# Performance work log

Hardware: AMD Instinct MI355X
Metric: run time of the kernel (lower is better)

Reference implementation:

```python
import jax, jax.numpy as jnp
import numpy as np

NUM_LEVELS = 3
K = 512
COMMIT = (0.25, 0.5, 1.0)
DECAY = 0.99
EPS = 1e-05


def setup_inputs() -> dict:
    key = jax.random.key(0)
    k1, k2, k3 = jax.random.split(key, 3)
    z_e = jax.random.normal(k1, (16, 4096, 1024), dtype=jnp.float32)
    codebooks = jax.random.normal(k2, (NUM_LEVELS, K, 1024), dtype=jnp.float32)
    ema_cluster = jnp.ones((NUM_LEVELS, K), dtype=jnp.float32)
    ema_w = jax.random.normal(k3, (NUM_LEVELS, K, 1024), dtype=jnp.float32)
    return {"z_e": z_e, "codebooks": codebooks, "ema_cluster": ema_cluster, "ema_w": ema_w}


def reference(z_e, codebooks, ema_cluster, ema_w):
    """Hierarchical residual VQ: 3 levels of cdist+argmin+gather, residual subtract,
    commitment loss, and EMA codebook update stats via scatter-add (segment_sum)."""
    B, T, D = z_e.shape
    flat = z_e.reshape(-1, D)  # [N, D]
    residual = flat
    z_q = jnp.zeros_like(flat)
    loss = jnp.zeros((), dtype=flat.dtype)
    idx_list = []
    new_codebooks = []

    for l in range(NUM_LEVELS):
        C = codebooks[l]  # [K, D]
        # squared euclidean distances [N, K] (expanded form, no NxKxD intermediate)
        d = (jnp.sum(residual * residual, axis=-1, keepdims=True)
             - 2.0 * residual @ C.T
             + jnp.sum(C * C, axis=-1))
        idx = jnp.argmin(d, axis=-1)  # [N] nearest code
        q = C[idx]  # gather [N, D]

        # commitment loss (EMA-style VQ: no gradient codebook loss)
        loss = loss + COMMIT[l] * jnp.mean((residual - jax.lax.stop_gradient(q)) ** 2)

        # EMA codebook update statistics (scatter-add, no grad)
        r_sg = jax.lax.stop_gradient(residual)
        counts = jax.ops.segment_sum(jnp.ones((r_sg.shape[0],), dtype=flat.dtype), idx, num_segments=K)
        sums = jax.ops.segment_sum(r_sg, idx, num_segments=K)  # [K, D]
        cs = DECAY * ema_cluster[l] + (1.0 - DECAY) * counts
        w = DECAY * ema_w[l] + (1.0 - DECAY) * sums
        n = jnp.sum(cs)
        cs_norm = (cs + EPS) / (n + K * EPS) * n  # laplace smoothing
        new_codebooks.append(w / cs_norm[:, None])

        residual = residual - q
        z_q = z_q + q
        idx_list.append(idx)

    # straight-through estimator
    z_q_st = flat + jax.lax.stop_gradient(z_q - flat)
    indices = jnp.stack(idx_list).reshape(NUM_LEVELS, B, T)
    return z_q_st.reshape(B, T, D), loss, indices, jnp.stack(new_codebooks)
```

## Files before the change

kernel.cpp:

```cpp
#include <hip/hip_runtime.h>

#define NPTS   65536
#define DIM    1024
#define NCODE  512
#define NLVL   3

#define ZQ_OFF   0
#define LOSS_OFF 67108864
#define IDX_OFF  67108865
#define CB_OFF   67305473

#define PB    128
#define CBCH  256
#define KS    64
#define NTHR2 512

typedef unsigned short u16;
typedef unsigned int   u32;
typedef __attribute__((ext_vector_type(8))) short short8;
typedef __attribute__((ext_vector_type(4))) float f32x4;

__device__ inline void merge_top2(float& v1, int& i1, float& v2, int& i2,
                                  float w1, int j1, float w2, int j2) {
    bool aFirst = (v1 < w1) || (v1 == w1 && i1 < j1);
    float t1v = aFirst ? v1 : w1; int t1i = aFirst ? i1 : j1;
    float c1v = aFirst ? v2 : w2; int c1i = aFirst ? i2 : j2;
    float c2v = aFirst ? w1 : v1; int c2i = aFirst ? j1 : i1;
    bool cFirst = (c1v < c2v) || (c1v == c2v && c1i < c2i);
    v1 = t1v; i1 = t1i;
    v2 = cFirst ? c1v : c2v;
    i2 = cFirst ? c1i : c2i;
}

__device__ inline u16 bf16_rne(float x) {
    u32 u = __float_as_uint(x);
    u32 r = u + 0x7fffu + ((u >> 16) & 1u);
    return (u16)(r >> 16);
}
__device__ inline float bf16_f(u16 h) { return __uint_as_float(((u32)h) << 16); }

__device__ inline void gload_lds16(const void* g, void* l) {
    __builtin_amdgcn_global_load_lds((const __attribute__((address_space(1))) void*)g,
                                     (__attribute__((address_space(3))) void*)l, 16, 0, 0);
}

__global__ __launch_bounds__(256) void cnorm_kernel(const float* __restrict__ cb,
                                                    float* __restrict__ cnorm) {
    __shared__ float sd[256];
    const int b = blockIdx.x;
    const int tid = threadIdx.x;
    const float4 v = *(const float4*)&cb[(size_t)b * DIM + tid * 4];
    sd[tid] = v.x*v.x + v.y*v.y + v.z*v.z + v.w*v.w;
    __syncthreads();
    for (int o = 128; o > 0; o >>= 1) { if (tid < o) sd[tid] += sd[tid+o]; __syncthreads(); }
    if (tid == 0) cnorm[b] = sd[0];
}

__global__ __launch_bounds__(256) void cvtcb_kernel(const float* __restrict__ cbs,
                                                    char* __restrict__ planes) {
    const int b = blockIdx.x;
    const int tid = threadIdx.x;
    const int l = b >> 9, k = b & 511;
    u16* ph = (u16*)(planes + (size_t)l * 2097152);
    u16* pl = ph + NCODE * DIM;
    const float4 v = *(const float4*)&cbs[(size_t)b * DIM + tid * 4];
    float xs[4] = {v.x, v.y, v.z, v.w};
    u16 hh[4], ll[4];
    #pragma unroll
    for (int e = 0; e < 4; ++e) {
        hh[e] = bf16_rne(xs[e]);
        ll[e] = bf16_rne(xs[e] - bf16_f(hh[e]));
    }
    *(ushort4*)&ph[(size_t)k * DIM + tid * 4] = make_ushort4(hh[0], hh[1], hh[2], hh[3]);
    *(ushort4*)&pl[(size_t)k * DIM + tid * 4] = make_ushort4(ll[0], ll[1], ll[2], ll[3]);
}

__global__ __launch_bounds__(512, 2) void level_kernel(
        const float* __restrict__ r_in,
        float* __restrict__ r_out,
        const float* __restrict__ cbf,
        const u16* __restrict__ cb_h,
        const u16* __restrict__ cb_l,
        const float* __restrict__ cnorm_l,
        float* __restrict__ out_idx_f,
        int*   __restrict__ ws_idx,
        float* __restrict__ loss_partial)
{
    __shared__ u16 sA[2][CBCH][KS];
    __shared__ u16 sB[2][PB][KS];
    __shared__ float s_cn[NCODE];
    __shared__ float4 s_top[4][PB];
    __shared__ int s_i1[PB], s_i2[PB], s_w[PB];
    __shared__ double s_ref[PB][2][2];
    __shared__ float s_red[NTHR2];

    const int tid  = threadIdx.x;
    const int lane = tid & 63;
    const int wid  = tid >> 6;
    const int wm   = wid >> 1;
    const int wn   = wid & 1;
    const int g    = lane >> 4;
    const int l15  = lane & 15;
    const int pbase = blockIdx.x * PB;

    u16* sAf = &sA[0][0][0];
    u16* sBf = &sB[0][0][0];

    s_cn[tid] = cnorm_l[tid];

    float bv1[4], bv2[4]; int bi1[4], bi2[4];
    #pragma unroll
    for (int i = 0; i < 4; ++i) { bv1[i] = 1e30f; bv2[i] = 1e30f; bi1[i] = 0; bi2[i] = 1; }

    const u16* srcp = (wid < 4) ? cb_h : cb_l;

    for (int ch = 0; ch < 2; ++ch) {
        const int cbase = ch * CBCH;
        f32x4 acc[4][4] = {};

        for (int ks0 = 0; ks0 < DIM; ks0 += KS) {
            __syncthreads();

            #pragma unroll
            for (int j = 0; j < 8; ++j) {
                const int cbk = wid * 512 + j * 64;
                const int c   = cbk + lane;
                const int cc  = c & 2047;
                const int row = cc >> 3, slot = cc & 7;
                const u16* gp = srcp + (size_t)(cbase + row) * DIM + ks0
                                + ((slot ^ (row & 7)) << 3);
                gload_lds16(gp, sAf + (size_t)cbk * 8);
            }

            #pragma unroll
            for (int j = 0; j < 2; ++j) {
                const int s = tid + j * 512;
                const int row = s >> 3, slot = s & 7;
                const float* gp = r_in + (size_t)(pbase + row) * DIM + ks0 + slot * 8;
                const float4 a0 = *(const float4*)gp;
                const float4 a1 = *(const float4*)(gp + 4);
                float xs[8] = {a0.x, a0.y, a0.z, a0.w, a1.x, a1.y, a1.z, a1.w};
                short8 h8, l8;
                #pragma unroll
                for (int e = 0; e < 8; ++e) {
                    const u16 hb = bf16_rne(xs[e]);
                    const u16 lb = bf16_rne(xs[e] - bf16_f(hb));
                    h8[e] = (short)hb; l8[e] = (short)lb;
                }
                const int woff = row * KS + ((slot ^ (row & 7)) << 3);
                *(short8*)(sBf + woff) = h8;
                *(short8*)(sBf + 8192 + woff) = l8;
            }
            asm volatile("s_waitcnt vmcnt(0)" ::: "memory");
            __syncthreads();

            #pragma unroll
            for (int ksub = 0; ksub < 2; ++ksub) {
                const int rsw = (((ksub << 2) + g) ^ (lane & 7)) << 3;
                short8 bh[4], bl[4];
                #pragma unroll
                for (int nf = 0; nf < 4; ++nf) {
                    const int row = wn * 64 + nf * 16 + l15;
                    bh[nf] = *(const short8*)(sBf + row * KS + rsw);
                    bl[nf] = *(const short8*)(sBf + 8192 + row * KS + rsw);
                }
                #pragma unroll
                for (int mf = 0; mf < 4; ++mf) {
                    const int row = wm * 64 + mf * 16 + l15;
                    const short8 ah = *(const short8*)(sAf + row * KS + rsw);
                    const short8 al = *(const short8*)(sAf + 16384 + row * KS + rsw);
                    #pragma unroll
                    for (int nf = 0; nf < 4; ++nf) {
                        acc[mf][nf] = __builtin_amdgcn_mfma_f32_16x16x32_bf16(ah, bh[nf], acc[mf][nf], 0, 0, 0);
                        acc[mf][nf] = __builtin_amdgcn_mfma_f32_16x16x32_bf16(ah, bl[nf], acc[mf][nf], 0, 0, 0);
                        acc[mf][nf] = __builtin_amdgcn_mfma_f32_16x16x32_bf16(al, bh[nf], acc[mf][nf], 0, 0, 0);
                    }
                }
            }
        }

        #pragma unroll
        for (int nf = 0; nf < 4; ++nf)
            #pragma unroll
            for (int mf = 0; mf < 4; ++mf)
                #pragma unroll
                for (int r = 0; r < 4; ++r) {
                    const int code = cbase + wm * 64 + mf * 16 + g * 4 + r;
                    const float sv = s_cn[code] - 2.0f * acc[mf][nf][r];
                    if (sv < bv1[nf])      { bv2[nf] = bv1[nf]; bi2[nf] = bi1[nf]; bv1[nf] = sv; bi1[nf] = code; }
                    else if (sv < bv2[nf]) { bv2[nf] = sv; bi2[nf] = code; }
                }
    }

    #pragma unroll
    for (int nf = 0; nf < 4; ++nf) {
        float v1 = bv1[nf], v2 = bv2[nf]; int i1 = bi1[nf], i2 = bi2[nf];
        #pragma unroll
        for (int m = 16; m < 64; m <<= 1) {
            const float w1 = __shfl_xor(v1, m); const int j1 = __shfl_xor(i1, m);
            const float w2 = __shfl_xor(v2, m); const int j2 = __shfl_xor(i2, m);
            merge_top2(v1, i1, v2, i2, w1, j1, w2, j2);
        }
        if (g == 0)
            s_top[wm][wn * 64 + nf * 16 + l15] =
                make_float4(v1, __int_as_float(i1), v2, __int_as_float(i2));
    }
    __syncthreads();

    if (tid < PB) {
        float4 t = s_top[0][tid];
        float v1 = t.x; int i1 = __float_as_int(t.y);
        float v2 = t.z; int i2 = __float_as_int(t.w);
        #pragma unroll
        for (int wmm = 1; wmm < 4; ++wmm) {
            const float4 u = s_top[wmm][tid];
            merge_top2(v1, i1, v2, i2, u.x, __float_as_int(u.y), u.z, __float_as_int(u.w));
        }
        s_i1[tid] = i1; s_i2[tid] = i2;
    }
    __syncthreads();

    {
        const int p = tid >> 2, cand = (tid >> 1) & 1, half = tid & 1;
        const int k = cand ? s_i2[p] : s_i1[p];
        const float* rr = r_in + (size_t)(pbase + p) * DIM + half * 512;
        const float* cr = cbf + (size_t)k * DIM + half * 512;
        double s = 0.0;
        for (int d = 0; d < 512; ++d) {
            const double c = (double)cr[d];
            const double r = (double)rr[d];
            s += c * (c - 2.0 * r);
        }
        s_ref[p][cand][half] = s;
    }
    __syncthreads();
    if (tid < PB) {
        const double sA_ = s_ref[tid][0][0] + s_ref[tid][0][1];
        const double sB_ = s_ref[tid][1][0] + s_ref[tid][1][1];
        const int iA = s_i1[tid], iB = s_i2[tid];
        const int w = (sB_ < sA_ || (sB_ == sA_ && iB < iA)) ? iB : iA;
        s_w[tid] = w;
        out_idx_f[pbase + tid] = (float)w;
        ws_idx[pbase + tid] = w;
    }
    __syncthreads();

    float lsum = 0.f;
    const int colb = (tid & 255) * 4;
    const int phh  = tid >> 8;
    for (int pp = 0; pp < PB; pp += 2) {
        const int p = pp + phh;
        const int w = s_w[p];
        const size_t off = (size_t)(pbase + p) * DIM + colb;
        const float4 rv = *(const float4*)&r_in[off];
        const float4 cv = *(const float4*)&cbf[(size_t)w * DIM + colb];
        float4 rn;
        rn.x = rv.x - cv.x; rn.y = rv.y - cv.y; rn.z = rv.z - cv.z; rn.w = rv.w - cv.w;
        if (r_out) *(float4*)&r_out[off] = rn;
        lsum += rn.x*rn.x + rn.y*rn.y + rn.z*rn.z + rn.w*rn.w;
    }
    s_red[tid] = lsum;
    __syncthreads();
    for (int o = 256; o > 0; o >>= 1) { if (tid < o) s_red[tid] += s_red[tid + o]; __syncthreads(); }
    if (tid == 0) loss_partial[blockIdx.x] = s_red[0];
}

#define SCHUNK 4096
__global__ __launch_bounds__(256) void sums_kernel(
        const int* __restrict__ idx, const float* __restrict__ src,
        const float* __restrict__ cb, int addC,
        float* __restrict__ sums_out, int* __restrict__ counts_out)
{
    __shared__ int s_idx[SCHUNK];
    __shared__ int s_list[SCHUNK];
    __shared__ int s_scan[256];
    const int k = blockIdx.x, tid = threadIdx.x;
    float4 acc = make_float4(0.f, 0.f, 0.f, 0.f);
    int nk = 0;
    for (int base = 0; base < NPTS; base += SCHUNK) {
        __syncthreads();
        for (int j = tid; j < SCHUNK; j += 256) s_idx[j] = idx[base + j];
        __syncthreads();
        int cnt = 0;
        const int S = SCHUNK / 256;
        #pragma unroll
        for (int j = 0; j < S; ++j) cnt += (s_idx[tid * S + j] == k);
        s_scan[tid] = cnt;
        __syncthreads();
        for (int off = 1; off < 256; off <<= 1) {
            int v = (tid >= off) ? s_scan[tid - off] : 0;
            __syncthreads();
            s_scan[tid] += v;
            __syncthreads();
        }
        const int total = s_scan[255];
        int pos = s_scan[tid] - cnt;
        for (int j = 0; j < S; ++j)
            if (s_idx[tid * S + j] == k) s_list[pos++] = base + tid * S + j;
        __syncthreads();
        for (int j = 0; j < total; ++j) {
            const int pid = s_list[j];
            float4 v = *(const float4*)&src[(size_t)pid * DIM + tid * 4];
            acc.x += v.x; acc.y += v.y; acc.z += v.z; acc.w += v.w;
        }
        nk += total;
    }
    if (addC) {
        float4 c = *(const float4*)&cb[(size_t)k * DIM + tid * 4];
        float fn = (float)nk;
        acc.x += fn * c.x; acc.y += fn * c.y; acc.z += fn * c.z; acc.w += fn * c.w;
    }
    *(float4*)&sums_out[(size_t)k * DIM + tid * 4] = acc;
    if (tid == 0) counts_out[k] = nk;
}

__global__ __launch_bounds__(256) void zq_kernel(const float* __restrict__ z_e,
                                                 const float* __restrict__ cb2,
                                                 const int* __restrict__ idx2,
                                                 float* __restrict__ zq) {
    const int total = NPTS * (DIM / 4);
    for (int i = blockIdx.x * 256 + threadIdx.x; i < total; i += gridDim.x * 256) {
        const size_t e = (size_t)i * 4;
        const int p = (int)(e >> 10);
        const int d = (int)(e & 1023);
        const int w = idx2[p];
        float4 z = *(const float4*)&z_e[e];
        float4 r = *(const float4*)&zq[e];
        float4 c = *(const float4*)&cb2[(size_t)w * DIM + d];
        float4 o;
        o.x = z.x - r.x + c.x; o.y = z.y - r.y + c.y;
        o.z = z.z - r.z + c.z; o.w = z.w - r.w + c.w;
        *(float4*)&zq[e] = o;
    }
}

__global__ __launch_bounds__(512) void nsum_kernel(const float* __restrict__ ec,
                                                   const int* __restrict__ counts,
                                                   float* __restrict__ n_ws) {
    __shared__ float sd[512];
    const int l = blockIdx.x, tid = threadIdx.x;
    sd[tid] = 0.99f * ec[l * NCODE + tid] + 0.01f * (float)counts[l * NCODE + tid];
    __syncthreads();
    for (int o = 256; o > 0; o >>= 1) { if (tid < o) sd[tid] += sd[tid+o]; __syncthreads(); }
    if (tid == 0) n_ws[l] = sd[0];
}

__global__ __launch_bounds__(256) void newcb_kernel(const float* __restrict__ ema_w,
                                                    const float* __restrict__ sums,
                                                    const float* __restrict__ ec,
                                                    const int* __restrict__ counts,
                                                    const float* __restrict__ n_ws,
                                                    float* __restrict__ out_cb) {
    const int b = blockIdx.x;
    const int tid = threadIdx.x;
    const int l = b >> 9;
    const float cs = 0.99f * ec[b] + 0.01f * (float)counts[b];
    const float n = n_ws[l];
    const float csn = (cs + 1e-5f) / (n + 512.0f * 1e-5f) * n;
    const size_t off = (size_t)b * DIM + tid * 4;
    float4 w = *(const float4*)&ema_w[off];
    float4 s4 = *(const float4*)&sums[off];
    float4 o;
    o.x = (0.99f * w.x + 0.01f * s4.x) / csn;
    o.y = (0.99f * w.y + 0.01f * s4.y) / csn;
    o.z = (0.99f * w.z + 0.01f * s4.z) / csn;
    o.w = (0.99f * w.w + 0.01f * s4.w) / csn;
    *(float4*)&out_cb[off] = o;
}

__global__ __launch_bounds__(256) void loss_kernel(const float* __restrict__ lp,
                                                   float* __restrict__ out_loss) {
    __shared__ double sd[256];
    const int tid = threadIdx.x;
    const double commit[3] = {0.25, 0.5, 1.0};
    double acc = 0.0;
    for (int l = 0; l < NLVL; ++l) {
        double s = 0.0;
        for (int j = tid; j < 512; j += 256) s += (double)lp[l * 512 + j];
        sd[tid] = s;
        __syncthreads();
        for (int o = 128; o > 0; o >>= 1) { if (tid < o) sd[tid] += sd[tid+o]; __syncthreads(); }
        if (tid == 0) acc += commit[l] * sd[0] / 67108864.0;
        __syncthreads();
    }
    if (tid == 0) *out_loss = (float)acc;
}

extern "C" void kernel_launch(void* const* d_in, const int* in_sizes, int n_in,
                              void* d_out, int out_size, void* d_ws, size_t ws_size,
                              hipStream_t stream) {
    const float* z_e   = (const float*)d_in[0];
    const float* cbs   = (const float*)d_in[1];
    const float* ema_c = (const float*)d_in[2];
    const float* ema_w = (const float*)d_in[3];
    float* out = (float*)d_out;

    char* ws = (char*)d_ws;
    int*   ws_idx = (int*)ws;
    float* cnorm  = (float*)(ws + 786432);
    int*   counts = (int*)(ws + 792576);
    float* lossp  = (float*)(ws + 798720);
    float* n_ws   = (float*)(ws + 811008);
    float* sums   = (float*)(ws + 811024);
    char*  planes = (char*)(ws + 811024);

    float* zq       = out + ZQ_OFF;
    float* out_loss = out + LOSS_OFF;
    float* out_idx  = out + IDX_OFF;
    float* out_cb   = out + CB_OFF;

    const float* cb0 = cbs;
    const float* cb1 = cbs + (size_t)1 * NCODE * DIM;
    const float* cb2 = cbs + (size_t)2 * NCODE * DIM;

    u16* ph0 = (u16*)(planes);                     u16* pl0 = ph0 + NCODE * DIM;
    u16* ph1 = (u16*)(planes + 2097152);           u16* pl1 = ph1 + NCODE * DIM;
    u16* ph2 = (u16*)(planes + 2 * 2097152);       u16* pl2 = ph2 + NCODE * DIM;

    cvtcb_kernel<<<NLVL * NCODE, 256, 0, stream>>>(cbs, planes);
    cnorm_kernel<<<NLVL * NCODE, 256, 0, stream>>>(cbs, cnorm);

    level_kernel<<<NPTS / PB, NTHR2, 0, stream>>>(z_e, zq, cb0, ph0, pl0, cnorm,
                                                  out_idx, ws_idx, lossp);
    sums_kernel<<<NCODE, 256, 0, stream>>>(ws_idx, z_e, nullptr, 0,
                                           sums, counts);
    level_kernel<<<NPTS / PB, NTHR2, 0, stream>>>(zq, zq, cb1, ph1, pl1, cnorm + NCODE,
                                                  out_idx + NPTS, ws_idx + NPTS, lossp + 512);
    sums_kernel<<<NCODE, 256, 0, stream>>>(ws_idx + NPTS, zq, cb1, 1,
                                           sums + (size_t)NCODE * DIM, counts + NCODE);
    level_kernel<<<NPTS / PB, NTHR2, 0, stream>>>(zq, nullptr, cb2, ph2, pl2, cnorm + 2 * NCODE,
                                                  out_idx + 2 * NPTS, ws_idx + 2 * NPTS, lossp + 1024);
    sums_kernel<<<NCODE, 256, 0, stream>>>(ws_idx + 2 * NPTS, zq, nullptr, 0,
                                           sums + (size_t)2 * NCODE * DIM, counts + 2 * NCODE);
    zq_kernel<<<4096, 256, 0, stream>>>(z_e, cb2, ws_idx + 2 * NPTS, zq);

    nsum_kernel<<<NLVL, 512, 0, stream>>>(ema_c, counts, n_ws);
    newcb_kernel<<<NLVL * NCODE, 256, 0, stream>>>(ema_w, sums, ema_c, counts, n_ws, out_cb);
    loss_kernel<<<1, 256, 0, stream>>>(lossp, out_loss);
}
```

Before: 2.872 ms.

## Halve K-slice depth, alias tail shared memory, and raise occupancy of level kernel

```diff
diff --git a/kernel.cpp b/kernel.cpp
--- a/kernel.cpp
+++ b/kernel.cpp
@@ -12,7 +12,7 @@
 
 #define PB    128
 #define CBCH  256
-#define KS    64
+#define KS    32
 #define NTHR2 512
 
 typedef unsigned short u16;
@@ -75,7 +75,7 @@
     *(ushort4*)&pl[(size_t)k * DIM + tid * 4] = make_ushort4(ll[0], ll[1], ll[2], ll[3]);
 }
 
-__global__ __launch_bounds__(512, 2) void level_kernel(
+__global__ __launch_bounds__(512, 4) void level_kernel(
         const float* __restrict__ r_in,
         float* __restrict__ r_out,
         const float* __restrict__ cbf,
@@ -86,13 +86,19 @@
         int*   __restrict__ ws_idx,
         float* __restrict__ loss_partial)
 {
-    __shared__ u16 sA[2][CBCH][KS];
-    __shared__ u16 sB[2][PB][KS];
+    __shared__ union {
+        struct {
+            u16 A[2][CBCH][KS];
+            u16 B[2][PB][KS];
+        } st;
+        struct {
+            float4 top[4][PB];
+            double ref[PB][2][2];
+            int    i1[PB], i2[PB], w[PB];
+            float  red[NTHR2];
+        } tl;
+    } sm;
     __shared__ float s_cn[NCODE];
-    __shared__ float4 s_top[4][PB];
-    __shared__ int s_i1[PB], s_i2[PB], s_w[PB];
-    __shared__ double s_ref[PB][2][2];
-    __shared__ float s_red[NTHR2];
 
     const int tid  = threadIdx.x;
     const int lane = tid & 63;
@@ -101,10 +107,11 @@
     const int wn   = wid & 1;
     const int g    = lane >> 4;
     const int l15  = lane & 15;
+    const int fr   = (l15 >> 1) & 3;
     const int pbase = blockIdx.x * PB;
 
-    u16* sAf = &sA[0][0][0];
-    u16* sBf = &sB[0][0][0];
+    u16* sAf = &sm.st.A[0][0][0];
+    u16* sBf = &sm.st.B[0][0][0];
 
     s_cn[tid] = cnorm_l[tid];
 
@@ -122,20 +129,17 @@
             __syncthreads();
 
             #pragma unroll
-            for (int j = 0; j < 8; ++j) {
-                const int cbk = wid * 512 + j * 64;
-                const int c   = cbk + lane;
-                const int cc  = c & 2047;
-                const int row = cc >> 3, slot = cc & 7;
+            for (int j = 0; j < 4; ++j) {
+                const int c   = wid * 256 + j * 64 + lane;
+                const int cc  = c & 1023;
+                const int row = cc >> 2, slot = cc & 3;
                 const u16* gp = srcp + (size_t)(cbase + row) * DIM + ks0
-                                + ((slot ^ (row & 7)) << 3);
-                gload_lds16(gp, sAf + (size_t)cbk * 8);
+                                + ((slot ^ ((row >> 1) & 3)) << 3);
+                gload_lds16(gp, sAf + (size_t)c * 8);
             }
 
-            #pragma unroll
-            for (int j = 0; j < 2; ++j) {
-                const int s = tid + j * 512;
-                const int row = s >> 3, slot = s & 7;
+            {
+                const int row = tid >> 2, slot = tid & 3;
                 const float* gp = r_in + (size_t)(pbase + row) * DIM + ks0 + slot * 8;
                 const float4 a0 = *(const float4*)gp;
                 const float4 a1 = *(const float4*)(gp + 4);
@@ -147,28 +151,27 @@
                     const u16 lb = bf16_rne(xs[e] - bf16_f(hb));
                     h8[e] = (short)hb; l8[e] = (short)lb;
                 }
-                const int woff = row * KS + ((slot ^ (row & 7)) << 3);
+                const int woff = row * KS + ((slot ^ ((row >> 1) & 3)) << 3);
                 *(short8*)(sBf + woff) = h8;
-                *(short8*)(sBf + 8192 + woff) = l8;
+                *(short8*)(sBf + 4096 + woff) = l8;
             }
             asm volatile("s_waitcnt vmcnt(0)" ::: "memory");
             __syncthreads();
 
-            #pragma unroll
-            for (int ksub = 0; ksub < 2; ++ksub) {
-                const int rsw = (((ksub << 2) + g) ^ (lane & 7)) << 3;
+            {
+                const int ksl = (g ^ fr) << 3;
                 short8 bh[4], bl[4];
                 #pragma unroll
                 for (int nf = 0; nf < 4; ++nf) {
                     const int row = wn * 64 + nf * 16 + l15;
-                    bh[nf] = *(const short8*)(sBf + row * KS + rsw);
-                    bl[nf] = *(const short8*)(sBf + 8192 + row * KS + rsw);
+                    bh[nf] = *(const short8*)(sBf + row * KS + ksl);
+                    bl[nf] = *(const short8*)(sBf + 4096 + row * KS + ksl);
                 }
                 #pragma unroll
                 for (int mf = 0; mf < 4; ++mf) {
                     const int row = wm * 64 + mf * 16 + l15;
-                    const short8 ah = *(const short8*)(sAf + row * KS + rsw);
-                    const short8 al = *(const short8*)(sAf + 16384 + row * KS + rsw);
+                    const short8 ah = *(const short8*)(sAf + row * KS + ksl);
+                    const short8 al = *(const short8*)(sAf + 8192 + row * KS + ksl);
                     #pragma unroll
                     for (int nf = 0; nf < 4; ++nf) {
                         acc[mf][nf] = __builtin_amdgcn_mfma_f32_16x16x32_bf16(ah, bh[nf], acc[mf][nf], 0, 0, 0);
@@ -192,6 +195,8 @@
                 }
     }
 
+    __syncthreads();
+
     #pragma unroll
     for (int nf = 0; nf < 4; ++nf) {
         float v1 = bv1[nf], v2 = bv2[nf]; int i1 = bi1[nf], i2 = bi2[nf];
@@ -202,44 +207,47 @@
             merge_top2(v1, i1, v2, i2, w1, j1, w2, j2);
         }
         if (g == 0)
-            s_top[wm][wn * 64 + nf * 16 + l15] =
+            sm.tl.top[wm][wn * 64 + nf * 16 + l15] =
                 make_float4(v1, __int_as_float(i1), v2, __int_as_float(i2));
     }
     __syncthreads();
 
     if (tid < PB) {
-        float4 t = s_top[0][tid];
+        float4 t = sm.tl.top[0][tid];
         float v1 = t.x; int i1 = __float_as_int(t.y);
         float v2 = t.z; int i2 = __float_as_int(t.w);
         #pragma unroll
         for (int wmm = 1; wmm < 4; ++wmm) {
-            const float4 u = s_top[wmm][tid];
+            const float4 u = sm.tl.top[wmm][tid];
             merge_top2(v1, i1, v2, i2, u.x, __float_as_int(u.y), u.z, __float_as_int(u.w));
         }
-        s_i1[tid] = i1; s_i2[tid] = i2;
+        sm.tl.i1[tid] = i1; sm.tl.i2[tid] = i2;
     }
     __syncthreads();
 
     {
         const int p = tid >> 2, cand = (tid >> 1) & 1, half = tid & 1;
-        const int k = cand ? s_i2[p] : s_i1[p];
-        const float* rr = r_in + (size_t)(pbase + p) * DIM + half * 512;
-        const float* cr = cbf + (size_t)k * DIM + half * 512;
-        double s = 0.0;
-        for (int d = 0; d < 512; ++d) {
-            const double c = (double)cr[d];
-            const double r = (double)rr[d];
-            s += c * (c - 2.0 * r);
-        }
-        s_ref[p][cand][half] = s;
+        const int k = cand ? sm.tl.i2[p] : sm.tl.i1[p];
+        const float4* rr = (const float4*)(r_in + (size_t)(pbase + p) * DIM + half * 512);
+        const float4* cr = (const float4*)(cbf + (size_t)k * DIM + half * 512);
+        double s0 = 0.0, s1 = 0.0, s2 = 0.0, s3 = 0.0;
+        for (int d = 0; d < 128; ++d) {
+            const float4 c4 = cr[d];
+            const float4 r4 = rr[d];
+            s0 += (double)c4.x * ((double)c4.x - 2.0 * (double)r4.x);
+            s1 += (double)c4.y * ((double)c4.y - 2.0 * (double)r4.y);
+            s2 += (double)c4.z * ((double)c4.z - 2.0 * (double)r4.z);
+            s3 += (double)c4.w * ((double)c4.w - 2.0 * (double)r4.w);
+        }
+        sm.tl.ref[p][cand][half] = (s0 + s1) + (s2 + s3);
     }
     __syncthreads();
     if (tid < PB) {
-        const double sA_ = s_ref[tid][0][0] + s_ref[tid][0][1];
-        const double sB_ = s_ref[tid][1][0] + s_ref[tid][1][1];
-        const int iA = s_i1[tid], iB = s_i2[tid];
+        const double sA_ = sm.tl.ref[tid][0][0] + sm.tl.ref[tid][0][1];
+        const double sB_ = sm.tl.ref[tid][1][0] + sm.tl.ref[tid][1][1];
+        const int iA = sm.tl.i1[tid], iB = sm.tl.i2[tid];
         const int w = (sB_ < sA_ || (sB_ == sA_ && iB < iA)) ? iB : iA;
-        s_w[tid] = w;
+        sm.tl.w[tid] = w;
         out_idx_f[pbase + tid] = (float)w;
         ws_idx[pbase + tid] = w;
     }
@@ -250,7 +258,7 @@
     const int phh  = tid >> 8;
     for (int pp = 0; pp < PB; pp += 2) {
         const int p = pp + phh;
-        const int w = s_w[p];
+        const int w = sm.tl.w[p];
         const size_t off = (size_t)(pbase + p) * DIM + colb;
         const float4 rv = *(const float4*)&r_in[off];
         const float4 cv = *(const float4*)&cbf[(size_t)w * DIM + colb];
@@ -259,10 +267,10 @@
         if (r_out) *(float4*)&r_out[off] = rn;
         lsum += rn.x*rn.x + rn.y*rn.y + rn.z*rn.z + rn.w*rn.w;
     }
-    s_red[tid] = lsum;
-    __syncthreads();
-    for (int o = 256; o > 0; o >>= 1) { if (tid < o) s_red[tid] += s_red[tid + o]; __syncthreads(); }
-    if (tid == 0) loss_partial[blockIdx.x] = s_red[0];
+    sm.tl.red[tid] = lsum;
+    __syncthreads();
+    for (int o = 256; o > 0; o >>= 1) { if (tid < o) sm.tl.red[tid] += sm.tl.red[tid + o]; __syncthreads(); }
+    if (tid == 0) loss_partial[blockIdx.x] = sm.tl.red[0];
 }
 
 #define SCHUNK 4096
```

New measurement: 2.648 ms. 1.08x faster.
